# Kernel tuning notes

Hardware: AMD Instinct MI355X
Metric: run time of the kernel (lower is better)

## Reference

```python
import jax, jax.numpy as jnp
import numpy as np

N0, N1, N2, N3 = 200000, 100000, 50000, 25000
E0, E1, E2 = 1600000, 800000, 400000
IN_DIM, HID = 16, 128


def setup_inputs() -> dict:
    key = jax.random.key(0)
    ks = jax.random.split(key, 12)
    inp = {
        "features": jax.random.normal(ks[0], (N0, IN_DIM), jnp.float32),
        "W_init": jax.random.normal(ks[1], (IN_DIM, HID), jnp.float32) / np.sqrt(IN_DIM),
        "b_init": jnp.zeros((HID,), jnp.float32),
        "W_self": jax.random.normal(ks[2], (HID, HID), jnp.float32) / np.sqrt(HID),
        "b_self": jnp.zeros((HID,), jnp.float32),
        "W_neigh": jax.random.normal(ks[3], (HID, HID), jnp.float32) / np.sqrt(HID),
        "b_neigh": jnp.zeros((HID,), jnp.float32),
        "src0": jax.random.randint(ks[4], (E0,), 0, N0, jnp.int32),
        "dst0": jax.random.randint(ks[5], (E0,), 0, N1, jnp.int32),
        "src1": jax.random.randint(ks[6], (E1,), 0, N1, jnp.int32),
        "dst1": jax.random.randint(ks[7], (E1,), 0, N2, jnp.int32),
        "src2": jax.random.randint(ks[8], (E2,), 0, N2, jnp.int32),
        "dst2": jax.random.randint(ks[9], (E2,), 0, N3, jnp.int32),
        "n1": N1, "n2": N2, "n3": N3,
    }
    return inp


def _mean_agg(h_src, src, dst, n_out):
    # gather messages along edges, segment-mean into dst nodes
    msg = h_src[src]                                             # [E, HID]
    agg = jax.ops.segment_sum(msg, dst, num_segments=n_out)      # [n_out, HID]
    cnt = jax.ops.segment_sum(jnp.ones_like(dst, jnp.float32), dst, num_segments=n_out)
    return agg / jnp.maximum(cnt, 1.0)[:, None]


def reference(features, W_init, b_init, W_self, b_self, W_neigh, b_neigh,
              src0, dst0, src1, dst1, src2, dst2, n1, n2, n3):
    # h = activation(fc_init(features))
    h = jax.nn.relu(features @ W_init + b_init)                  # [N0, HID]
    blocks = [(src0, dst0, n1), (src1, dst1, n2), (src2, dst2, n3)]
    depth = len(blocks)
    for i, (src, dst, n_out) in enumerate(blocks):
        h_neigh = _mean_agg(h, src, dst, n_out)
        # SAGEConv mean, combine_type='sum': fc_self(h_dst) + fc_neigh(mean_neigh)
        h = (h[:n_out] @ W_self + b_self) + (h_neigh @ W_neigh + b_neigh)
        if i != depth - 1:
            h = jax.nn.relu(h)
    return h                                                     # [N3, HID]
```

## Files before the change

### kernel.cpp

```cpp
#include <hip/hip_runtime.h>

#define HID 128
#define CAP 64
#define NCB 49
#define TILE 1024
#define CCAP0 40960
#define CCAP1 20480
#define CCAP2 10240

typedef __attribute__((ext_vector_type(2))) _Float16 h2v;
typedef __attribute__((ext_vector_type(8))) _Float16 f16x8;
typedef __attribute__((ext_vector_type(4))) float f32x4;

__global__ __launch_bounds__(256) void h0_and_bin(
        const float* __restrict__ feat, const float* __restrict__ W_init,
        const float* __restrict__ b_init, _Float16* __restrict__ h0, int M, int nh0blk,
        const int* __restrict__ src0, const int* __restrict__ dst0, int E0,
        const int* __restrict__ src1, const int* __restrict__ dst1, int E1,
        const int* __restrict__ src2, const int* __restrict__ dst2, int E2,
        int* __restrict__ gcur,
        int* __restrict__ buf0, int* __restrict__ buf1, int* __restrict__ buf2,
        int nb0, int nb1, int nb2) {
    __shared__ int hist[NCB];
    __shared__ int gbase[NCB];
    const int nbTot = nb0 + nb1 + nb2;
    if (blockIdx.x < (unsigned)nbTot) {
        const int* src; const int* dst; int E, SH, lb, nblk, ccap; int* buf; int* cur;
        int b = blockIdx.x;
        if (b < nb0)             { src = src0; dst = dst0; E = E0; SH = 11; lb = b;             nblk = nb0; buf = buf0; cur = gcur;           ccap = CCAP0; }
        else if (b < nb0 + nb1)  { src = src1; dst = dst1; E = E1; SH = 10; lb = b - nb0;       nblk = nb1; buf = buf1; cur = gcur + NCB;     ccap = CCAP1; }
        else                     { src = src2; dst = dst2; E = E2; SH = 9;  lb = b - nb0 - nb1; nblk = nb2; buf = buf2; cur = gcur + 2 * NCB; ccap = CCAP2; }
        const int ntile = (E + TILE - 1) / TILE;
        for (int t = lb; t < ntile; t += nblk) {
            const int base = t * TILE;
            const int n = min(TILE, E - base);
            for (int i = threadIdx.x; i < NCB; i += 256) hist[i] = 0;
            __syncthreads();
            int eb[4], er[4], ee[4];
#pragma unroll
            for (int k = 0; k < 4; k++) {
                int idx = k * 256 + threadIdx.x;
                eb[k] = -1;
                if (idx < n) {
                    int d = dst[base + idx], s = src[base + idx];
                    int bb = d >> SH;
                    eb[k] = bb;
                    ee[k] = ((d - (bb << SH)) << 18) | s;
                    er[k] = atomicAdd(&hist[bb], 1);
                }
            }
            __syncthreads();
            if (threadIdx.x < NCB)
                gbase[threadIdx.x] = atomicAdd(&cur[threadIdx.x], hist[threadIdx.x]);
            __syncthreads();
#pragma unroll
            for (int k = 0; k < 4; k++) {
                if (eb[k] >= 0) {
                    int pos = gbase[eb[k]] + er[k];
                    if (pos < ccap) buf[(size_t)eb[k] * ccap + pos] = ee[k];
                }
            }
            __syncthreads();
        }
        return;
    }
    const int hbid = blockIdx.x - nbTot;
    const int tid  = threadIdx.x;
    const int lane = tid & 63;
    const int wave = tid >> 6;
    const int ln15 = lane & 15;
    const int quad = lane >> 4;

    f16x8 Bf[2];
    float bias[2];
#pragma unroll
    for (int cc = 0; cc < 2; cc++) {
        int n = (wave * 2 + cc) * 16 + ln15;
        bias[cc] = b_init[n];
        f16x8 b;
#pragma unroll
        for (int jj = 0; jj < 8; jj++) {
            int k = quad * 8 + jj;
            b[jj] = (k < 16) ? (_Float16)W_init[k * HID + n] : (_Float16)0.f;
        }
        Bf[cc] = b;
    }

    for (int row0 = hbid * 16; row0 < M; row0 += nh0blk * 16) {
        const int arow = row0 + ln15;
        f16x8 A = {0, 0, 0, 0, 0, 0, 0, 0};
        if (arow < M && quad < 2) {
            const float* p = feat + (size_t)arow * 16 + quad * 8;
            float4 v0 = *(const float4*)p;
            float4 v1 = *(const float4*)(p + 4);
            A[0] = (_Float16)v0.x; A[1] = (_Float16)v0.y;
            A[2] = (_Float16)v0.z; A[3] = (_Float16)v0.w;
            A[4] = (_Float16)v1.x; A[5] = (_Float16)v1.y;
            A[6] = (_Float16)v1.z; A[7] = (_Float16)v1.w;
        }
        f32x4 acc0 = {0.f, 0.f, 0.f, 0.f};
        f32x4 acc1 = {0.f, 0.f, 0.f, 0.f};
        acc0 = __builtin_amdgcn_mfma_f32_16x16x32_f16(A, Bf[0], acc0, 0, 0, 0);
        acc1 = __builtin_amdgcn_mfma_f32_16x16x32_f16(A, Bf[1], acc1, 0, 0, 0);
#pragma unroll
        for (int cc = 0; cc < 2; cc++) {
            int col = (wave * 2 + cc) * 16 + ln15;
            f32x4 acc = cc ? acc1 : acc0;
#pragma unroll
            for (int r = 0; r < 4; r++) {
                int row = row0 + quad * 4 + r;
                if (row < M)
                    h0[(size_t)row * HID + col] = (_Float16)fmaxf(acc[r] + bias[cc], 0.f);
            }
        }
    }
}

__global__ __launch_bounds__(1024) void refine_coarse(
        const int* __restrict__ buf0, const int* __restrict__ buf1, const int* __restrict__ buf2,
        const int* __restrict__ gcur, int* __restrict__ csrcur,
        int N1v, int N2v, int N3v,
        int* __restrict__ csr0, int* __restrict__ off0, int* __restrict__ cnt0,
        int* __restrict__ csr1, int* __restrict__ off1, int* __restrict__ cnt1,
        int* __restrict__ csr2, int* __restrict__ off2, int* __restrict__ cnt2) {
    __shared__ int hist[2048];
    __shared__ int loff[2048];
    __shared__ int wsum[16];
    __shared__ int blkbase;
    const int tid = threadIdx.x;
    const int gb = blockIdx.x;
    const int* buf; int* csr; int* off; int* cnt; int* ccur;
    int SH, N, bb, ccap, m;
    if (gb < NCB)          { buf = buf0; csr = csr0; off = off0; cnt = cnt0; ccur = csrcur;     SH = 11; N = N1v; bb = gb;           ccap = CCAP0; }
    else if (gb < 2 * NCB) { buf = buf1; csr = csr1; off = off1; cnt = cnt1; ccur = csrcur + 1; SH = 10; N = N2v; bb = gb - NCB;     ccap = CCAP1; }
    else                   { buf = buf2; csr = csr2; off = off2; cnt = cnt2; ccur = csrcur + 2; SH = 9;  N = N3v; bb = gb - 2 * NCB; ccap = CCAP2; }
    m = min(gcur[gb], ccap);
    const int* __restrict__ seg = buf + (size_t)bb * ccap;
    const int nb_d = 1 << SH;
    for (int i = tid; i < 2048; i += 1024) hist[i] = 0;
    __syncthreads();
    for (int i = tid; i < m; i += 1024)
        atomicAdd(&hist[((unsigned)seg[i]) >> 18], 1);
    __syncthreads();
    int v0 = hist[2 * tid], v1 = hist[2 * tid + 1];
    int s = v0 + v1;
    int lane = tid & 63;
    int incl = s;
#pragma unroll
    for (int d = 1; d < 64; d <<= 1) {
        int up = __shfl_up(incl, d, 64);
        if (lane >= d) incl += up;
    }
    if (lane == 63) wsum[tid >> 6] = incl;
    __syncthreads();
    if (tid == 0) {
        int acc = 0;
#pragma unroll
        for (int i = 0; i < 16; i++) { int w = wsum[i]; wsum[i] = acc; acc += w; }
        blkbase = atomicAdd(ccur, acc);
    }
    __syncthreads();
    int base = blkbase + wsum[tid >> 6] + (incl - s);
    loff[2 * tid] = base;
    loff[2 * tid + 1] = base + v0;
    const int dbase = bb << SH;
    {
        int dl0 = 2 * tid, dl1 = 2 * tid + 1;
        if (dl0 < nb_d && dbase + dl0 < N) { off[dbase + dl0] = base;      cnt[dbase + dl0] = v0; }
        if (dl1 < nb_d && dbase + dl1 < N) { off[dbase + dl1] = base + v0; cnt[dbase + dl1] = v1; }
    }
    __syncthreads();
    for (int i = tid; i < 2048; i += 1024) hist[i] = 0;
    __syncthreads();
    for (int i = tid; i < m; i += 1024) {
        int e = seg[i];
        int dl = ((unsigned)e) >> 18;
        int p = atomicAdd(&hist[dl], 1);
        csr[loff[dl] + p] = e & 0x3FFFF;
    }
}

__device__ __forceinline__ void acc8(float* s, uint4 u) {
    union { uint4 u; h2v p[4]; } w; w.u = u;
#pragma unroll
    for (int q = 0; q < 4; q++) {
        s[2 * q]     += (float)w.p[q][0];
        s[2 * q + 1] += (float)w.p[q][1];
    }
}

__global__ __launch_bounds__(256) void gather_mean(
        const _Float16* __restrict__ h,
        const int* __restrict__ csr,
        const int* __restrict__ off,
        const int* __restrict__ cnt,
        _Float16* __restrict__ Xm,
        int n_out) {
    const int g = threadIdx.x >> 4;
    const int c = threadIdx.x & 15;
    const int node = blockIdx.x * 16 + g;
    if (node >= n_out) return;
    int deg = min(cnt[node], CAP);
    const int* __restrict__ sl = csr + off[node];
    float s[8] = {0.f, 0.f, 0.f, 0.f, 0.f, 0.f, 0.f, 0.f};
    int e = 0;
    for (; e + 8 <= deg; e += 8) {
        uint4 R[8];
#pragma unroll
        for (int k = 0; k < 8; k++)
            R[k] = *(const uint4*)(h + (size_t)sl[e + k] * HID + c * 8);
#pragma unroll
        for (int k = 0; k < 8; k++) acc8(s, R[k]);
    }
    if (e + 4 <= deg) {
        uint4 R[4];
#pragma unroll
        for (int k = 0; k < 4; k++)
            R[k] = *(const uint4*)(h + (size_t)sl[e + k] * HID + c * 8);
#pragma unroll
        for (int k = 0; k < 4; k++) acc8(s, R[k]);
        e += 4;
    }
    for (; e < deg; e++)
        acc8(s, *(const uint4*)(h + (size_t)sl[e] * HID + c * 8));
    float inv = 1.0f / (float)max(deg, 1);
    union { uint4 u; h2v p[4]; } mo;
#pragma unroll
    for (int q = 0; q < 4; q++)
        mo.p[q] = (h2v){(_Float16)(s[2 * q] * inv), (_Float16)(s[2 * q + 1] * inv)};
    *(uint4*)(Xm + (size_t)node * HID + c * 8) = mo.u;
}

template <bool RELU, typename OutT>
__global__ __launch_bounds__(256) void mfma_combine2(
        const _Float16* __restrict__ Hself, const _Float16* __restrict__ Xm,
        const float* __restrict__ Wself, const float* __restrict__ bself,
        const float* __restrict__ Wneigh, const float* __restrict__ bneigh,
        OutT* __restrict__ out, int M) {
    const int tid  = threadIdx.x;
    const int lane = tid & 63;
    const int wave = tid >> 6;
    const int ln15 = lane & 15;
    const int quad = lane >> 4;

    f16x8 Bf[2][8];
    float bias[2];
#pragma unroll
    for (int cc = 0; cc < 2; cc++) {
        int n = (wave * 2 + cc) * 16 + ln15;
        bias[cc] = bself[n] + bneigh[n];
#pragma unroll
        for (int s = 0; s < 8; s++) {
            f16x8 b;
#pragma unroll
            for (int jj = 0; jj < 8; jj++) {
                int k = s * 32 + quad * 8 + jj;
                float w = (k < HID) ? Wself[k * HID + n] : Wneigh[(k - HID) * HID + n];
                b[jj] = (_Float16)w;
            }
            Bf[cc][s] = b;
        }
    }

    for (int row0 = blockIdx.x * 16; row0 < M; row0 += gridDim.x * 16) {
        const int arow = row0 + ln15;
        const bool inb = arow < M;
        const _Float16* aps = Hself + (size_t)arow * HID + quad * 8;
        const _Float16* apm = Xm    + (size_t)arow * HID + quad * 8;
        f32x4 acc0 = {0.f, 0.f, 0.f, 0.f};
        f32x4 acc1 = {0.f, 0.f, 0.f, 0.f};
#pragma unroll
        for (int s = 0; s < 8; s++) {
            f16x8 A;
            if (inb) A = (s < 4) ? *(const f16x8*)(aps + s * 32)
                                 : *(const f16x8*)(apm + (s - 4) * 32);
            else     A = (f16x8){0, 0, 0, 0, 0, 0, 0, 0};
            acc0 = __builtin_amdgcn_mfma_f32_16x16x32_f16(A, Bf[0][s], acc0, 0, 0, 0);
            acc1 = __builtin_amdgcn_mfma_f32_16x16x32_f16(A, Bf[1][s], acc1, 0, 0, 0);
        }
#pragma unroll
        for (int cc = 0; cc < 2; cc++) {
            int col = (wave * 2 + cc) * 16 + ln15;
            f32x4 acc = cc ? acc1 : acc0;
#pragma unroll
            for (int r = 0; r < 4; r++) {
                int row = row0 + quad * 4 + r;
                if (row < M) {
                    float v = acc[r] + bias[cc];
                    if (RELU) v = fmaxf(v, 0.f);
                    out[(size_t)row * HID + col] = (OutT)v;
                }
            }
        }
    }
}

extern "C" void kernel_launch(void* const* d_in, const int* in_sizes, int n_in,
                              void* d_out, int out_size, void* d_ws, size_t ws_size,
                              hipStream_t stream) {
    const float* feat    = (const float*)d_in[0];
    const float* W_init  = (const float*)d_in[1];
    const float* b_init  = (const float*)d_in[2];
    const float* W_self  = (const float*)d_in[3];
    const float* b_self  = (const float*)d_in[4];
    const float* W_neigh = (const float*)d_in[5];
    const float* b_neigh = (const float*)d_in[6];
    const int* src0 = (const int*)d_in[7];
    const int* dst0 = (const int*)d_in[8];
    const int* src1 = (const int*)d_in[9];
    const int* dst1 = (const int*)d_in[10];
    const int* src2 = (const int*)d_in[11];
    const int* dst2 = (const int*)d_in[12];

    const int N0 = in_sizes[0] / 16;
    const int E0 = in_sizes[7];
    const int E1 = in_sizes[9];
    const int E2 = in_sizes[11];
    const int N1 = 100000, N2 = 50000, N3 = 25000;

    _Float16* h0 = (_Float16*)d_ws;
    _Float16* hA = h0 + (size_t)N0 * HID;
    int* csr0 = (int*)(hA + (size_t)N1 * HID);
    int* csr1 = csr0 + E0;
    int* csr2 = csr1 + E1;
    int* off0 = csr2 + E2;
    int* off1 = off0 + N1;
    int* off2 = off1 + N2;
    int* cnt0 = off2 + N3;
    int* cnt1 = cnt0 + N1;
    int* cnt2 = cnt1 + N2;
    int* gcur = cnt2 + N3;
    int* csrcur = gcur + 3 * NCB;
    int* buf0 = csrcur + 3;
    int* buf1 = buf0 + (size_t)NCB * CCAP0;
    int* buf2 = buf1 + (size_t)NCB * CCAP1;
    _Float16* Xm = (_Float16*)buf0;
    _Float16* hB = h0;

    hipMemsetAsync(gcur, 0, (3 * NCB + 3) * sizeof(int), stream);

    const int nb0 = 768, nb1 = 384, nb2 = 192, nh0blk = 3136;
    h0_and_bin<<<nb0 + nb1 + nb2 + nh0blk, 256, 0, stream>>>(
        feat, W_init, b_init, h0, N0, nh0blk,
        src0, dst0, E0, src1, dst1, E1, src2, dst2, E2,
        gcur, buf0, buf1, buf2, nb0, nb1, nb2);
    refine_coarse<<<3 * NCB, 1024, 0, stream>>>(
        buf0, buf1, buf2, gcur, csrcur, N1, N2, N3,
        csr0, off0, cnt0, csr1, off1, cnt1, csr2, off2, cnt2);

    gather_mean<<<(N1 + 15) / 16, 256, 0, stream>>>(h0, csr0, off0, cnt0, Xm, N1);
    mfma_combine2<true, _Float16><<<min((N1 + 15) / 16, 1568), 256, 0, stream>>>(
        h0, Xm, W_self, b_self, W_neigh, b_neigh, hA, N1);
    gather_mean<<<(N2 + 15) / 16, 256, 0, stream>>>(hA, csr1, off1, cnt1, Xm, N2);
    mfma_combine2<true, _Float16><<<min((N2 + 15) / 16, 1568), 256, 0, stream>>>(
        hA, Xm, W_self, b_self, W_neigh, b_neigh, hB, N2);
    gather_mean<<<(N3 + 15) / 16, 256, 0, stream>>>(hB, csr2, off2, cnt2, Xm, N3);
    mfma_combine2<false, float><<<min((N3 + 15) / 16, 1568), 256, 0, stream>>>(
        hB, Xm, W_self, b_self, W_neigh, b_neigh, (float*)d_out, N3);
}
```

Baseline: 402.5 us.

## Build CSR via global count, scan and atomic scatter instead of bucket sort

Replaces the two-stage coarse-bucket binning plus per-bucket LDS refine with a three-kernel CSR build. The first kernel counts in-degrees with global atomics, the second does an exclusive-scan into cursors, and the third scatters src ids into CSR slots with returning global atomicSub. The initial feature projection also moves from MFMA to plain fp32 FMA per output column, fused into the counting kernel. This removes the large staging buffers and one full pass over the edges. The cost is millions of random returning global atomics and nondeterministic neighbor order within each row.

```diff
diff --git a/kernel.cpp b/kernel.cpp
--- a/kernel.cpp
+++ b/kernel.cpp
@@ -2,148 +2,84 @@
 
 #define HID 128
 #define CAP 64
-#define NCB 49
-#define TILE 1024
-#define CCAP0 40960
-#define CCAP1 20480
-#define CCAP2 10240
 
 typedef __attribute__((ext_vector_type(2))) _Float16 h2v;
 typedef __attribute__((ext_vector_type(8))) _Float16 f16x8;
 typedef __attribute__((ext_vector_type(4))) float f32x4;
 
-__global__ __launch_bounds__(256) void h0_and_bin(
+__global__ __launch_bounds__(256) void h0_and_count(
         const float* __restrict__ feat, const float* __restrict__ W_init,
-        const float* __restrict__ b_init, _Float16* __restrict__ h0, int M, int nh0blk,
-        const int* __restrict__ src0, const int* __restrict__ dst0, int E0,
-        const int* __restrict__ src1, const int* __restrict__ dst1, int E1,
-        const int* __restrict__ src2, const int* __restrict__ dst2, int E2,
-        int* __restrict__ gcur,
-        int* __restrict__ buf0, int* __restrict__ buf1, int* __restrict__ buf2,
-        int nb0, int nb1, int nb2) {
-    __shared__ int hist[NCB];
-    __shared__ int gbase[NCB];
-    const int nbTot = nb0 + nb1 + nb2;
-    if (blockIdx.x < (unsigned)nbTot) {
-        const int* src; const int* dst; int E, SH, lb, nblk, ccap; int* buf; int* cur;
-        int b = blockIdx.x;
-        if (b < nb0)             { src = src0; dst = dst0; E = E0; SH = 11; lb = b;             nblk = nb0; buf = buf0; cur = gcur;           ccap = CCAP0; }
-        else if (b < nb0 + nb1)  { src = src1; dst = dst1; E = E1; SH = 10; lb = b - nb0;       nblk = nb1; buf = buf1; cur = gcur + NCB;     ccap = CCAP1; }
-        else                     { src = src2; dst = dst2; E = E2; SH = 9;  lb = b - nb0 - nb1; nblk = nb2; buf = buf2; cur = gcur + 2 * NCB; ccap = CCAP2; }
-        const int ntile = (E + TILE - 1) / TILE;
-        for (int t = lb; t < ntile; t += nblk) {
-            const int base = t * TILE;
-            const int n = min(TILE, E - base);
-            for (int i = threadIdx.x; i < NCB; i += 256) hist[i] = 0;
-            __syncthreads();
-            int eb[4], er[4], ee[4];
-#pragma unroll
-            for (int k = 0; k < 4; k++) {
-                int idx = k * 256 + threadIdx.x;
-                eb[k] = -1;
-                if (idx < n) {
-                    int d = dst[base + idx], s = src[base + idx];
-                    int bb = d >> SH;
-                    eb[k] = bb;
-                    ee[k] = ((d - (bb << SH)) << 18) | s;
-                    er[k] = atomicAdd(&hist[bb], 1);
-                }
+        const float* __restrict__ b_init, _Float16* __restrict__ h0, int M,
+        int nCnt, int nH0,
+        const int* __restrict__ dst0, int E0,
+        const int* __restrict__ dst1, int E1,
+        const int* __restrict__ dst2, int E2,
+        int* __restrict__ cnt0, int* __restrict__ cnt1, int* __restrict__ cnt2) {
+    const int b = blockIdx.x;
+    if (b < nCnt) {
+        const int nc0 = nCnt / 2, nc1 = nCnt / 4;
+        const int* dst; int* cnt; int E, lb, nb;
+        if (b < nc0)            { dst = dst0; cnt = cnt0; E = E0; lb = b;             nb = nc0; }
+        else if (b < nc0 + nc1) { dst = dst1; cnt = cnt1; E = E1; lb = b - nc0;       nb = nc1; }
+        else                    { dst = dst2; cnt = cnt2; E = E2; lb = b - nc0 - nc1; nb = nCnt - nc0 - nc1; }
+        const int n4 = E >> 2;
+        for (int i = lb * 256 + threadIdx.x; i < n4; i += nb * 256) {
+            int4 d = ((const int4*)dst)[i];
+            atomicAdd(&cnt[d.x], 1);
+            atomicAdd(&cnt[d.y], 1);
+            atomicAdd(&cnt[d.z], 1);
+            atomicAdd(&cnt[d.w], 1);
+        }
+        if (lb == 0) {
+            int t = (E & ~3) + threadIdx.x;
+            if (t < E) atomicAdd(&cnt[dst[t]], 1);
+        }
+        return;
+    }
+    const int hb = b - nCnt;
+    const int j  = threadIdx.x & 127;
+    const int rl = threadIdx.x >> 7;
+    float Wc[16];
+#pragma unroll
+    for (int k = 0; k < 16; k++) Wc[k] = W_init[k * HID + j];
+    const float bi = b_init[j];
+    for (int r0 = hb * 8; r0 < M; r0 += nH0 * 8) {
+        float4 F[4][4];
+#pragma unroll
+        for (int u = 0; u < 4; u++) {
+            int row = r0 + u * 2 + rl;
+            if (row < M) {
+                const float4* p = (const float4*)(feat + (size_t)row * 16);
+                F[u][0] = p[0]; F[u][1] = p[1]; F[u][2] = p[2]; F[u][3] = p[3];
             }
-            __syncthreads();
-            if (threadIdx.x < NCB)
-                gbase[threadIdx.x] = atomicAdd(&cur[threadIdx.x], hist[threadIdx.x]);
-            __syncthreads();
-#pragma unroll
-            for (int k = 0; k < 4; k++) {
-                if (eb[k] >= 0) {
-                    int pos = gbase[eb[k]] + er[k];
-                    if (pos < ccap) buf[(size_t)eb[k] * ccap + pos] = ee[k];
-                }
-            }
-            __syncthreads();
-        }
-        return;
-    }
-    const int hbid = blockIdx.x - nbTot;
-    const int tid  = threadIdx.x;
-    const int lane = tid & 63;
-    const int wave = tid >> 6;
-    const int ln15 = lane & 15;
-    const int quad = lane >> 4;
-
-    f16x8 Bf[2];
-    float bias[2];
-#pragma unroll
-    for (int cc = 0; cc < 2; cc++) {
-        int n = (wave * 2 + cc) * 16 + ln15;
-        bias[cc] = b_init[n];
-        f16x8 b;
-#pragma unroll
-        for (int jj = 0; jj < 8; jj++) {
-            int k = quad * 8 + jj;
-            b[jj] = (k < 16) ? (_Float16)W_init[k * HID + n] : (_Float16)0.f;
-        }
-        Bf[cc] = b;
-    }
-
-    for (int row0 = hbid * 16; row0 < M; row0 += nh0blk * 16) {
-        const int arow = row0 + ln15;
-        f16x8 A = {0, 0, 0, 0, 0, 0, 0, 0};
-        if (arow < M && quad < 2) {
-            const float* p = feat + (size_t)arow * 16 + quad * 8;
-            float4 v0 = *(const float4*)p;
-            float4 v1 = *(const float4*)(p + 4);
-            A[0] = (_Float16)v0.x; A[1] = (_Float16)v0.y;
-            A[2] = (_Float16)v0.z; A[3] = (_Float16)v0.w;
-            A[4] = (_Float16)v1.x; A[5] = (_Float16)v1.y;
-            A[6] = (_Float16)v1.z; A[7] = (_Float16)v1.w;
-        }
-        f32x4 acc0 = {0.f, 0.f, 0.f, 0.f};
-        f32x4 acc1 = {0.f, 0.f, 0.f, 0.f};
-        acc0 = __builtin_amdgcn_mfma_f32_16x16x32_f16(A, Bf[0], acc0, 0, 0, 0);
-        acc1 = __builtin_amdgcn_mfma_f32_16x16x32_f16(A, Bf[1], acc1, 0, 0, 0);
-#pragma unroll
-        for (int cc = 0; cc < 2; cc++) {
-            int col = (wave * 2 + cc) * 16 + ln15;
-            f32x4 acc = cc ? acc1 : acc0;
-#pragma unroll
-            for (int r = 0; r < 4; r++) {
-                int row = row0 + quad * 4 + r;
-                if (row < M)
-                    h0[(size_t)row * HID + col] = (_Float16)fmaxf(acc[r] + bias[cc], 0.f);
-            }
-        }
-    }
-}
-
-__global__ __launch_bounds__(1024) void refine_coarse(
-        const int* __restrict__ buf0, const int* __restrict__ buf1, const int* __restrict__ buf2,
-        const int* __restrict__ gcur, int* __restrict__ csrcur,
-        int N1v, int N2v, int N3v,
-        int* __restrict__ csr0, int* __restrict__ off0, int* __restrict__ cnt0,
-        int* __restrict__ csr1, int* __restrict__ off1, int* __restrict__ cnt1,
-        int* __restrict__ csr2, int* __restrict__ off2, int* __restrict__ cnt2) {
-    __shared__ int hist[2048];
-    __shared__ int loff[2048];
-    __shared__ int wsum[16];
-    __shared__ int blkbase;
+        }
+#pragma unroll
+        for (int u = 0; u < 4; u++) {
+            int row = r0 + u * 2 + rl;
+            if (row >= M) continue;
+            const float* f = (const float*)&F[u][0];
+            float a = bi;
+#pragma unroll
+            for (int k = 0; k < 16; k++) a = fmaf(f[k], Wc[k], a);
+            h0[(size_t)row * HID + j] = (_Float16)fmaxf(a, 0.f);
+        }
+    }
+}
+
+__global__ __launch_bounds__(1024) void scan_cur(
+        const int* __restrict__ cnt0, const int* __restrict__ cnt1, const int* __restrict__ cnt2,
+        int* __restrict__ cur0, int* __restrict__ cur1, int* __restrict__ cur2,
+        int N1v, int N2v, int N3v, int nb1, int nb2, int* __restrict__ gb) {
+    const int b = blockIdx.x;
+    const int* cnt; int* cur; int N, lb; int* g;
+    if (b < nb1)            { cnt = cnt0; cur = cur0; N = N1v; lb = b;             g = gb;     }
+    else if (b < nb1 + nb2) { cnt = cnt1; cur = cur1; N = N2v; lb = b - nb1;       g = gb + 1; }
+    else                    { cnt = cnt2; cur = cur2; N = N3v; lb = b - nb1 - nb2; g = gb + 2; }
     const int tid = threadIdx.x;
-    const int gb = blockIdx.x;
-    const int* buf; int* csr; int* off; int* cnt; int* ccur;
-    int SH, N, bb, ccap, m;
-    if (gb < NCB)          { buf = buf0; csr = csr0; off = off0; cnt = cnt0; ccur = csrcur;     SH = 11; N = N1v; bb = gb;           ccap = CCAP0; }
-    else if (gb < 2 * NCB) { buf = buf1; csr = csr1; off = off1; cnt = cnt1; ccur = csrcur + 1; SH = 10; N = N2v; bb = gb - NCB;     ccap = CCAP1; }
-    else                   { buf = buf2; csr = csr2; off = off2; cnt = cnt2; ccur = csrcur + 2; SH = 9;  N = N3v; bb = gb - 2 * NCB; ccap = CCAP2; }
-    m = min(gcur[gb], ccap);
-    const int* __restrict__ seg = buf + (size_t)bb * ccap;
-    const int nb_d = 1 << SH;
-    for (int i = tid; i < 2048; i += 1024) hist[i] = 0;
-    __syncthreads();
-    for (int i = tid; i < m; i += 1024)
-        atomicAdd(&hist[((unsigned)seg[i]) >> 18], 1);
-    __syncthreads();
-    int v0 = hist[2 * tid], v1 = hist[2 * tid + 1];
-    int s = v0 + v1;
+    const int base = lb * 4096 + tid * 4;
+    int v[4]; int s = 0;
+#pragma unroll
+    for (int k = 0; k < 4; k++) { v[k] = (base + k < N) ? cnt[base + k] : 0; s += v[k]; }
     int lane = tid & 63;
     int incl = s;
 #pragma unroll
@@ -151,32 +87,52 @@
         int up = __shfl_up(incl, d, 64);
         if (lane >= d) incl += up;
     }
+    __shared__ int wsum[16];
+    __shared__ int bbase;
     if (lane == 63) wsum[tid >> 6] = incl;
     __syncthreads();
     if (tid == 0) {
         int acc = 0;
 #pragma unroll
         for (int i = 0; i < 16; i++) { int w = wsum[i]; wsum[i] = acc; acc += w; }
-        blkbase = atomicAdd(ccur, acc);
+        bbase = atomicAdd(g, acc);
     }
     __syncthreads();
-    int base = blkbase + wsum[tid >> 6] + (incl - s);
-    loff[2 * tid] = base;
-    loff[2 * tid + 1] = base + v0;
-    const int dbase = bb << SH;
-    {
-        int dl0 = 2 * tid, dl1 = 2 * tid + 1;
-        if (dl0 < nb_d && dbase + dl0 < N) { off[dbase + dl0] = base;      cnt[dbase + dl0] = v0; }
-        if (dl1 < nb_d && dbase + dl1 < N) { off[dbase + dl1] = base + v0; cnt[dbase + dl1] = v1; }
-    }
-    __syncthreads();
-    for (int i = tid; i < 2048; i += 1024) hist[i] = 0;
-    __syncthreads();
-    for (int i = tid; i < m; i += 1024) {
-        int e = seg[i];
-        int dl = ((unsigned)e) >> 18;
-        int p = atomicAdd(&hist[dl], 1);
-        csr[loff[dl] + p] = e & 0x3FFFF;
+    int run = bbase + wsum[tid >> 6] + (incl - s);
+#pragma unroll
+    for (int k = 0; k < 4; k++) {
+        run += v[k];
+        if (base + k < N) cur[base + k] = run;
+    }
+}
+
+__global__ __launch_bounds__(256) void scatter_csr(
+        const int* __restrict__ src0, const int* __restrict__ dst0, int E0,
+        const int* __restrict__ src1, const int* __restrict__ dst1, int E1,
+        const int* __restrict__ src2, const int* __restrict__ dst2, int E2,
+        int* __restrict__ cur0, int* __restrict__ cur1, int* __restrict__ cur2,
+        int* __restrict__ csr0, int* __restrict__ csr1, int* __restrict__ csr2,
+        int nc0, int nc1, int nc2) {
+    const int b = blockIdx.x;
+    const int *src, *dst; int *cur, *csr; int E, lb, nb;
+    if (b < nc0)            { src = src0; dst = dst0; cur = cur0; csr = csr0; E = E0; lb = b;             nb = nc0; }
+    else if (b < nc0 + nc1) { src = src1; dst = dst1; cur = cur1; csr = csr1; E = E1; lb = b - nc0;       nb = nc1; }
+    else                    { src = src2; dst = dst2; cur = cur2; csr = csr2; E = E2; lb = b - nc0 - nc1; nb = nc2; }
+    const int n4 = E >> 2;
+    for (int i = lb * 256 + threadIdx.x; i < n4; i += nb * 256) {
+        int4 d = ((const int4*)dst)[i];
+        int4 s = ((const int4*)src)[i];
+        int p0 = atomicSub(&cur[d.x], 1) - 1; csr[p0] = s.x;
+        int p1 = atomicSub(&cur[d.y], 1) - 1; csr[p1] = s.y;
+        int p2 = atomicSub(&cur[d.z], 1) - 1; csr[p2] = s.z;
+        int p3 = atomicSub(&cur[d.w], 1) - 1; csr[p3] = s.w;
+    }
+    if (lb == 0) {
+        int t = (E & ~3) + threadIdx.x;
+        if (t < E) {
+            int p = atomicSub(&cur[dst[t]], 1) - 1;
+            csr[p] = src[t];
+        }
     }
 }
 
@@ -319,42 +275,43 @@
     const int N1 = 100000, N2 = 50000, N3 = 25000;
 
     _Float16* h0 = (_Float16*)d_ws;
-    _Float16* hA = h0 + (size_t)N0 * HID;
-    int* csr0 = (int*)(hA + (size_t)N1 * HID);
-    int* csr1 = csr0 + E0;
+    _Float16* Xm = h0 + (size_t)N0 * HID;
+    int* csr1 = (int*)(Xm + (size_t)N1 * HID);
     int* csr2 = csr1 + E1;
-    int* off0 = csr2 + E2;
-    int* off1 = off0 + N1;
-    int* off2 = off1 + N2;
-    int* cnt0 = off2 + N3;
+    int* cnt0 = csr2 + E2;
     int* cnt1 = cnt0 + N1;
     int* cnt2 = cnt1 + N2;
-    int* gcur = cnt2 + N3;
-    int* csrcur = gcur + 3 * NCB;
-    int* buf0 = csrcur + 3;
-    int* buf1 = buf0 + (size_t)NCB * CCAP0;
-    int* buf2 = buf1 + (size_t)NCB * CCAP1;
-    _Float16* Xm = (_Float16*)buf0;
+    int* gb   = cnt2 + N3;
+    int* cur0 = gb + 16;
+    int* cur1 = cur0 + N1;
+    int* cur2 = cur1 + N2;
+    int* csr0 = cur2 + N3;
+    _Float16* hA = (_Float16*)csr0;
     _Float16* hB = h0;
 
-    hipMemsetAsync(gcur, 0, (3 * NCB + 3) * sizeof(int), stream);
-
-    const int nb0 = 768, nb1 = 384, nb2 = 192, nh0blk = 3136;
-    h0_and_bin<<<nb0 + nb1 + nb2 + nh0blk, 256, 0, stream>>>(
-        feat, W_init, b_init, h0, N0, nh0blk,
+    hipMemsetAsync(cnt0, 0, (size_t)(N1 + N2 + N3 + 16) * sizeof(int), stream);
+
+    const int nCnt = 896, nH0 = 3200;
+    h0_and_count<<<nCnt + nH0, 256, 0, stream>>>(
+        feat, W_init, b_init, h0, N0, nCnt, nH0,
+        dst0, E0, dst1, E1, dst2, E2, cnt0, cnt1, cnt2);
+
+    const int nb1 = (N1 + 4095) / 4096, nb2 = (N2 + 4095) / 4096, nb3 = (N3 + 4095) / 4096;
+    scan_cur<<<nb1 + nb2 + nb3, 1024, 0, stream>>>(
+        cnt0, cnt1, cnt2, cur0, cur1, cur2, N1, N2, N3, nb1, nb2, gb);
+
+    const int ns0 = 768, ns1 = 384, ns2 = 192;
+    scatter_csr<<<ns0 + ns1 + ns2, 256, 0, stream>>>(
         src0, dst0, E0, src1, dst1, E1, src2, dst2, E2,
-        gcur, buf0, buf1, buf2, nb0, nb1, nb2);
-    refine_coarse<<<3 * NCB, 1024, 0, stream>>>(
-        buf0, buf1, buf2, gcur, csrcur, N1, N2, N3,
-        csr0, off0, cnt0, csr1, off1, cnt1, csr2, off2, cnt2);
-
-    gather_mean<<<(N1 + 15) / 16, 256, 0, stream>>>(h0, csr0, off0, cnt0, Xm, N1);
+        cur0, cur1, cur2, csr0, csr1, csr2, ns0, ns1, ns2);
+
+    gather_mean<<<(N1 + 15) / 16, 256, 0, stream>>>(h0, csr0, cur0, cnt0, Xm, N1);
     mfma_combine2<true, _Float16><<<min((N1 + 15) / 16, 1568), 256, 0, stream>>>(
         h0, Xm, W_self, b_self, W_neigh, b_neigh, hA, N1);
-    gather_mean<<<(N2 + 15) / 16, 256, 0, stream>>>(hA, csr1, off1, cnt1, Xm, N2);
+    gather_mean<<<(N2 + 15) / 16, 256, 0, stream>>>(hA, csr1, cur1, cnt1, Xm, N2);
     mfma_combine2<true, _Float16><<<min((N2 + 15) / 16, 1568), 256, 0, stream>>>(
         hA, Xm, W_self, b_self, W_neigh, b_neigh, hB, N2);
-    gather_mean<<<(N3 + 15) / 16, 256, 0, stream>>>(hB, csr2, off2, cnt2, Xm, N3);
+    gather_mean<<<(N3 + 15) / 16, 256, 0, stream>>>(hB, csr2, cur2, cnt2, Xm, N3);
     mfma_combine2<false, float><<<min((N3 + 15) / 16, 1568), 256, 0, stream>>>(
         hB, Xm, W_self, b_self, W_neigh, b_neigh, (float*)d_out, N3);
 }
```

Result: slower. 695.4 us (+72.8%).

## Fuse neighbor gather-mean into MFMA combine kernel via shared-memory tile

Applied to the files above, without the earlier changes.

Merges the per-layer gather_mean and mfma_combine2 kernels into one persistent gather_combine kernel. Each block gathers the neighbor mean for 16 nodes into a shared-memory tile and feeds it straight to the MFMA matmul, so the Xm intermediate never goes to global memory and three launches are removed. It also doubles the edge-binning tile to 2048 edges per iteration. The trade-off is that the fused kernel serializes gather and matmul phases within each block with extra barriers and caps the grid at 1568 blocks, which may lower the number of gathers in flight.

```diff
diff --git a/kernel.cpp b/kernel.cpp
--- a/kernel.cpp
+++ b/kernel.cpp
@@ -3,7 +3,7 @@
 #define HID 128
 #define CAP 64
 #define NCB 49
-#define TILE 1024
+#define TILE 2048
 #define CCAP0 40960
 #define CCAP1 20480
 #define CCAP2 10240
@@ -36,9 +36,9 @@
             const int n = min(TILE, E - base);
             for (int i = threadIdx.x; i < NCB; i += 256) hist[i] = 0;
             __syncthreads();
-            int eb[4], er[4], ee[4];
-#pragma unroll
-            for (int k = 0; k < 4; k++) {
+            int eb[8], er[8], ee[8];
+#pragma unroll
+            for (int k = 0; k < 8; k++) {
                 int idx = k * 256 + threadIdx.x;
                 eb[k] = -1;
                 if (idx < n) {
@@ -54,7 +54,7 @@
                 gbase[threadIdx.x] = atomicAdd(&cur[threadIdx.x], hist[threadIdx.x]);
             __syncthreads();
 #pragma unroll
-            for (int k = 0; k < 4; k++) {
+            for (int k = 0; k < 8; k++) {
                 if (eb[k] >= 0) {
                     int pos = gbase[eb[k]] + er[k];
                     if (pos < ccap) buf[(size_t)eb[k] * ccap + pos] = ee[k];
@@ -189,59 +189,23 @@
     }
 }
 
-__global__ __launch_bounds__(256) void gather_mean(
+template <bool RELU, typename OutT>
+__global__ __launch_bounds__(256) void gather_combine(
         const _Float16* __restrict__ h,
         const int* __restrict__ csr,
         const int* __restrict__ off,
         const int* __restrict__ cnt,
-        _Float16* __restrict__ Xm,
-        int n_out) {
-    const int g = threadIdx.x >> 4;
-    const int c = threadIdx.x & 15;
-    const int node = blockIdx.x * 16 + g;
-    if (node >= n_out) return;
-    int deg = min(cnt[node], CAP);
-    const int* __restrict__ sl = csr + off[node];
-    float s[8] = {0.f, 0.f, 0.f, 0.f, 0.f, 0.f, 0.f, 0.f};
-    int e = 0;
-    for (; e + 8 <= deg; e += 8) {
-        uint4 R[8];
-#pragma unroll
-        for (int k = 0; k < 8; k++)
-            R[k] = *(const uint4*)(h + (size_t)sl[e + k] * HID + c * 8);
-#pragma unroll
-        for (int k = 0; k < 8; k++) acc8(s, R[k]);
-    }
-    if (e + 4 <= deg) {
-        uint4 R[4];
-#pragma unroll
-        for (int k = 0; k < 4; k++)
-            R[k] = *(const uint4*)(h + (size_t)sl[e + k] * HID + c * 8);
-#pragma unroll
-        for (int k = 0; k < 4; k++) acc8(s, R[k]);
-        e += 4;
-    }
-    for (; e < deg; e++)
-        acc8(s, *(const uint4*)(h + (size_t)sl[e] * HID + c * 8));
-    float inv = 1.0f / (float)max(deg, 1);
-    union { uint4 u; h2v p[4]; } mo;
-#pragma unroll
-    for (int q = 0; q < 4; q++)
-        mo.p[q] = (h2v){(_Float16)(s[2 * q] * inv), (_Float16)(s[2 * q + 1] * inv)};
-    *(uint4*)(Xm + (size_t)node * HID + c * 8) = mo.u;
-}
-
-template <bool RELU, typename OutT>
-__global__ __launch_bounds__(256) void mfma_combine2(
-        const _Float16* __restrict__ Hself, const _Float16* __restrict__ Xm,
         const float* __restrict__ Wself, const float* __restrict__ bself,
         const float* __restrict__ Wneigh, const float* __restrict__ bneigh,
-        OutT* __restrict__ out, int M) {
+        OutT* __restrict__ out, int M, int nblk) {
+    __shared__ uint4 Xt[16][17];
     const int tid  = threadIdx.x;
     const int lane = tid & 63;
     const int wave = tid >> 6;
     const int ln15 = lane & 15;
     const int quad = lane >> 4;
+    const int g = tid >> 4;
+    const int c = tid & 15;
 
     f16x8 Bf[2][8];
     float bias[2];
@@ -262,36 +226,77 @@
         }
     }
 
-    for (int row0 = blockIdx.x * 16; row0 < M; row0 += gridDim.x * 16) {
-        const int arow = row0 + ln15;
-        const bool inb = arow < M;
-        const _Float16* aps = Hself + (size_t)arow * HID + quad * 8;
-        const _Float16* apm = Xm    + (size_t)arow * HID + quad * 8;
-        f32x4 acc0 = {0.f, 0.f, 0.f, 0.f};
-        f32x4 acc1 = {0.f, 0.f, 0.f, 0.f};
-#pragma unroll
-        for (int s = 0; s < 8; s++) {
-            f16x8 A;
-            if (inb) A = (s < 4) ? *(const f16x8*)(aps + s * 32)
-                                 : *(const f16x8*)(apm + (s - 4) * 32);
-            else     A = (f16x8){0, 0, 0, 0, 0, 0, 0, 0};
-            acc0 = __builtin_amdgcn_mfma_f32_16x16x32_f16(A, Bf[0][s], acc0, 0, 0, 0);
-            acc1 = __builtin_amdgcn_mfma_f32_16x16x32_f16(A, Bf[1][s], acc1, 0, 0, 0);
-        }
-#pragma unroll
-        for (int cc = 0; cc < 2; cc++) {
-            int col = (wave * 2 + cc) * 16 + ln15;
-            f32x4 acc = cc ? acc1 : acc0;
-#pragma unroll
-            for (int r = 0; r < 4; r++) {
-                int row = row0 + quad * 4 + r;
-                if (row < M) {
-                    float v = acc[r] + bias[cc];
-                    if (RELU) v = fmaxf(v, 0.f);
-                    out[(size_t)row * HID + col] = (OutT)v;
-                }
-            }
-        }
+    for (int row0 = blockIdx.x * 16; row0 < M; row0 += nblk * 16) {
+        {
+            const int node = row0 + g;
+            union { uint4 u; h2v p[4]; } mo;
+            mo.u = (uint4){0, 0, 0, 0};
+            if (node < M) {
+                int deg = min(cnt[node], CAP);
+                const int* __restrict__ sl = csr + off[node];
+                float s[8] = {0.f, 0.f, 0.f, 0.f, 0.f, 0.f, 0.f, 0.f};
+                int e = 0;
+                for (; e + 8 <= deg; e += 8) {
+                    uint4 R[8];
+#pragma unroll
+                    for (int k = 0; k < 8; k++)
+                        R[k] = *(const uint4*)(h + (size_t)sl[e + k] * HID + c * 8);
+#pragma unroll
+                    for (int k = 0; k < 8; k++) acc8(s, R[k]);
+                }
+                if (e + 4 <= deg) {
+                    uint4 R[4];
+#pragma unroll
+                    for (int k = 0; k < 4; k++)
+                        R[k] = *(const uint4*)(h + (size_t)sl[e + k] * HID + c * 8);
+#pragma unroll
+                    for (int k = 0; k < 4; k++) acc8(s, R[k]);
+                    e += 4;
+                }
+                for (; e < deg; e++)
+                    acc8(s, *(const uint4*)(h + (size_t)sl[e] * HID + c * 8));
+                float inv = 1.0f / (float)max(deg, 1);
+#pragma unroll
+                for (int q = 0; q < 4; q++)
+                    mo.p[q] = (h2v){(_Float16)(s[2 * q] * inv), (_Float16)(s[2 * q + 1] * inv)};
+            }
+            Xt[g][c] = mo.u;
+        }
+        __syncthreads();
+        {
+            const int arow = row0 + ln15;
+            const bool inb = arow < M;
+            const _Float16* aps = h + (size_t)arow * HID + quad * 8;
+            f32x4 acc0 = {0.f, 0.f, 0.f, 0.f};
+            f32x4 acc1 = {0.f, 0.f, 0.f, 0.f};
+#pragma unroll
+            for (int s = 0; s < 8; s++) {
+                f16x8 A;
+                if (s < 4) {
+                    if (inb) A = *(const f16x8*)(aps + s * 32);
+                    else     A = (f16x8){0, 0, 0, 0, 0, 0, 0, 0};
+                } else {
+                    A = *(const f16x8*)&Xt[ln15][(s - 4) * 4 + quad];
+                }
+                acc0 = __builtin_amdgcn_mfma_f32_16x16x32_f16(A, Bf[0][s], acc0, 0, 0, 0);
+                acc1 = __builtin_amdgcn_mfma_f32_16x16x32_f16(A, Bf[1][s], acc1, 0, 0, 0);
+            }
+#pragma unroll
+            for (int cc = 0; cc < 2; cc++) {
+                int col = (wave * 2 + cc) * 16 + ln15;
+                f32x4 acc = cc ? acc1 : acc0;
+#pragma unroll
+                for (int r = 0; r < 4; r++) {
+                    int row = row0 + quad * 4 + r;
+                    if (row < M) {
+                        float v = acc[r] + bias[cc];
+                        if (RELU) v = fmaxf(v, 0.f);
+                        out[(size_t)row * HID + col] = (OutT)v;
+                    }
+                }
+            }
+        }
+        __syncthreads();
     }
 }
 
@@ -334,7 +339,6 @@
     int* buf0 = csrcur + 3;
     int* buf1 = buf0 + (size_t)NCB * CCAP0;
     int* buf2 = buf1 + (size_t)NCB * CCAP1;
-    _Float16* Xm = (_Float16*)buf0;
     _Float16* hB = h0;
 
     hipMemsetAsync(gcur, 0, (3 * NCB + 3) * sizeof(int), stream);
@@ -348,13 +352,19 @@
         buf0, buf1, buf2, gcur, csrcur, N1, N2, N3,
         csr0, off0, cnt0, csr1, off1, cnt1, csr2, off2, cnt2);
 
-    gather_mean<<<(N1 + 15) / 16, 256, 0, stream>>>(h0, csr0, off0, cnt0, Xm, N1);
-    mfma_combine2<true, _Float16><<<min((N1 + 15) / 16, 1568), 256, 0, stream>>>(
-        h0, Xm, W_self, b_self, W_neigh, b_neigh, hA, N1);
-    gather_mean<<<(N2 + 15) / 16, 256, 0, stream>>>(hA, csr1, off1, cnt1, Xm, N2);
-    mfma_combine2<true, _Float16><<<min((N2 + 15) / 16, 1568), 256, 0, stream>>>(
-        hA, Xm, W_self, b_self, W_neigh, b_neigh, hB, N2);
-    gather_mean<<<(N3 + 15) / 16, 256, 0, stream>>>(hB, csr2, off2, cnt2, Xm, N3);
-    mfma_combine2<false, float><<<min((N3 + 15) / 16, 1568), 256, 0, stream>>>(
-        hB, Xm, W_self, b_self, W_neigh, b_neigh, (float*)d_out, N3);
-}
+    {
+        int g = min((N1 + 15) / 16, 1568);
+        gather_combine<true, _Float16><<<g, 256, 0, stream>>>(
+            h0, csr0, off0, cnt0, W_self, b_self, W_neigh, b_neigh, hA, N1, g);
+    }
+    {
+        int g = min((N2 + 15) / 16, 1568);
+        gather_combine<true, _Float16><<<g, 256, 0, stream>>>(
+            hA, csr1, off1, cnt1, W_self, b_self, W_neigh, b_neigh, hB, N2, g);
+    }
+    {
+        int g = min((N3 + 15) / 16, 1568);
+        gather_combine<false, float><<<g, 256, 0, stream>>>(
+            hB, csr2, off2, cnt2, W_self, b_self, W_neigh, b_neigh, (float*)d_out, N3, g);
+    }
+}
```

Result: no change. 408.1 us (+1.4%).

## Split edge binning into finer sub-buckets and fuse CSR refine with h0

Applied to the files above, without the earlier changes.

Edge binning now uses 512-node coarse buckets, each split into 8 per-block sub-buckets, with 2048-edge tiles. The CSR refine step therefore runs on 343 smaller 512-thread blocks instead of 147 1024-thread blocks, and contention on the global bucket cursors is lower. The h0 input projection moves out of the binning kernel and into the refine kernel so it overlaps with the refine work. The combine layers now write in place into one feature buffer, with a block barrier added before the stores. The fixed per-sub-bucket capacity can silently drop edges if a sub-bucket overflows.

```diff
diff --git a/kernel.cpp b/kernel.cpp
--- a/kernel.cpp
+++ b/kernel.cpp
@@ -2,72 +2,141 @@
 
 #define HID 128
 #define CAP 64
-#define NCB 49
-#define TILE 1024
-#define CCAP0 40960
-#define CCAP1 20480
-#define CCAP2 10240
+#define SHB 9
+#define NCB0 196
+#define NCB1 98
+#define NCB2 49
+#define SUB 8
+#define CS 1280
+#define TILE 2048
 
 typedef __attribute__((ext_vector_type(2))) _Float16 h2v;
 typedef __attribute__((ext_vector_type(8))) _Float16 f16x8;
 typedef __attribute__((ext_vector_type(4))) float f32x4;
 
-__global__ __launch_bounds__(256) void h0_and_bin(
-        const float* __restrict__ feat, const float* __restrict__ W_init,
-        const float* __restrict__ b_init, _Float16* __restrict__ h0, int M, int nh0blk,
+__global__ __launch_bounds__(256) void bin_coarse(
         const int* __restrict__ src0, const int* __restrict__ dst0, int E0,
         const int* __restrict__ src1, const int* __restrict__ dst1, int E1,
         const int* __restrict__ src2, const int* __restrict__ dst2, int E2,
         int* __restrict__ gcur,
         int* __restrict__ buf0, int* __restrict__ buf1, int* __restrict__ buf2,
         int nb0, int nb1, int nb2) {
-    __shared__ int hist[NCB];
-    __shared__ int gbase[NCB];
-    const int nbTot = nb0 + nb1 + nb2;
-    if (blockIdx.x < (unsigned)nbTot) {
-        const int* src; const int* dst; int E, SH, lb, nblk, ccap; int* buf; int* cur;
-        int b = blockIdx.x;
-        if (b < nb0)             { src = src0; dst = dst0; E = E0; SH = 11; lb = b;             nblk = nb0; buf = buf0; cur = gcur;           ccap = CCAP0; }
-        else if (b < nb0 + nb1)  { src = src1; dst = dst1; E = E1; SH = 10; lb = b - nb0;       nblk = nb1; buf = buf1; cur = gcur + NCB;     ccap = CCAP1; }
-        else                     { src = src2; dst = dst2; E = E2; SH = 9;  lb = b - nb0 - nb1; nblk = nb2; buf = buf2; cur = gcur + 2 * NCB; ccap = CCAP2; }
-        const int ntile = (E + TILE - 1) / TILE;
-        for (int t = lb; t < ntile; t += nblk) {
-            const int base = t * TILE;
-            const int n = min(TILE, E - base);
-            for (int i = threadIdx.x; i < NCB; i += 256) hist[i] = 0;
-            __syncthreads();
-            int eb[4], er[4], ee[4];
-#pragma unroll
-            for (int k = 0; k < 4; k++) {
-                int idx = k * 256 + threadIdx.x;
-                eb[k] = -1;
-                if (idx < n) {
-                    int d = dst[base + idx], s = src[base + idx];
-                    int bb = d >> SH;
-                    eb[k] = bb;
-                    ee[k] = ((d - (bb << SH)) << 18) | s;
-                    er[k] = atomicAdd(&hist[bb], 1);
-                }
-            }
-            __syncthreads();
-            if (threadIdx.x < NCB)
-                gbase[threadIdx.x] = atomicAdd(&cur[threadIdx.x], hist[threadIdx.x]);
-            __syncthreads();
-#pragma unroll
-            for (int k = 0; k < 4; k++) {
-                if (eb[k] >= 0) {
-                    int pos = gbase[eb[k]] + er[k];
-                    if (pos < ccap) buf[(size_t)eb[k] * ccap + pos] = ee[k];
-                }
-            }
-            __syncthreads();
+    __shared__ int hist[NCB0];
+    __shared__ int gbase[NCB0];
+    const int* src; const int* dst; int E, lb, nblk, ncb; int* buf; int* cur;
+    int b = blockIdx.x;
+    if (b < nb0)             { src = src0; dst = dst0; E = E0; lb = b;             nblk = nb0; buf = buf0; cur = gcur;                          ncb = NCB0; }
+    else if (b < nb0 + nb1)  { src = src1; dst = dst1; E = E1; lb = b - nb0;       nblk = nb1; buf = buf1; cur = gcur + NCB0 * SUB;             ncb = NCB1; }
+    else                     { src = src2; dst = dst2; E = E2; lb = b - nb0 - nb1; nblk = nb2; buf = buf2; cur = gcur + (NCB0 + NCB1) * SUB;    ncb = NCB2; }
+    const int sub = lb & (SUB - 1);
+    const int ntile = (E + TILE - 1) / TILE;
+    for (int t = lb; t < ntile; t += nblk) {
+        const int base = t * TILE;
+        const int n = min(TILE, E - base);
+        for (int i = threadIdx.x; i < ncb; i += 256) hist[i] = 0;
+        __syncthreads();
+        int eb[8], er[8], ee[8];
+#pragma unroll
+        for (int k = 0; k < 8; k++) {
+            int idx = k * 256 + threadIdx.x;
+            eb[k] = -1;
+            if (idx < n) {
+                int d = dst[base + idx], s = src[base + idx];
+                int bb = d >> SHB;
+                eb[k] = bb;
+                ee[k] = ((d & 511) << 18) | s;
+                er[k] = atomicAdd(&hist[bb], 1);
+            }
+        }
+        __syncthreads();
+        for (int i = threadIdx.x; i < ncb; i += 256)
+            gbase[i] = atomicAdd(&cur[i * SUB + sub], hist[i]);
+        __syncthreads();
+#pragma unroll
+        for (int k = 0; k < 8; k++) {
+            if (eb[k] >= 0) {
+                int pos = gbase[eb[k]] + er[k];
+                if (pos < CS) buf[((size_t)eb[k] * SUB + sub) * CS + pos] = ee[k];
+            }
+        }
+        __syncthreads();
+    }
+}
+
+__global__ __launch_bounds__(512) void refine_h0(
+        const int* __restrict__ buf0, const int* __restrict__ buf1, const int* __restrict__ buf2,
+        const int* __restrict__ gcur, int* __restrict__ csrcur,
+        int N1v, int N2v, int N3v, int nRef,
+        int* __restrict__ csr0, int* __restrict__ off0, int* __restrict__ cnt0,
+        int* __restrict__ csr1, int* __restrict__ off1, int* __restrict__ cnt1,
+        int* __restrict__ csr2, int* __restrict__ off2, int* __restrict__ cnt2,
+        const float* __restrict__ feat, const float* __restrict__ W_init,
+        const float* __restrict__ b_init, _Float16* __restrict__ h0, int M, int nh0) {
+    __shared__ int hist[512];
+    __shared__ int loff[512];
+    __shared__ int wsum[8];
+    __shared__ int blkbase;
+    const int tid = threadIdx.x;
+    if (blockIdx.x < (unsigned)nRef) {
+        const int gb = blockIdx.x;
+        const int* buf; int* csr; int* off; int* cnt; int* ccur; const int* cur;
+        int N, bb;
+        if (gb < NCB0)            { buf = buf0; csr = csr0; off = off0; cnt = cnt0; ccur = csrcur;     cur = gcur;                       N = N1v; bb = gb; }
+        else if (gb < NCB0 + NCB1){ buf = buf1; csr = csr1; off = off1; cnt = cnt1; ccur = csrcur + 1; cur = gcur + NCB0 * SUB;          N = N2v; bb = gb - NCB0; }
+        else                      { buf = buf2; csr = csr2; off = off2; cnt = cnt2; ccur = csrcur + 2; cur = gcur + (NCB0 + NCB1) * SUB; N = N3v; bb = gb - NCB0 - NCB1; }
+        int m[SUB];
+#pragma unroll
+        for (int j = 0; j < SUB; j++) m[j] = min(cur[bb * SUB + j], CS);
+        hist[tid] = 0;
+        __syncthreads();
+#pragma unroll
+        for (int j = 0; j < SUB; j++) {
+            const int* __restrict__ seg = buf + ((size_t)bb * SUB + j) * CS;
+            for (int i = tid; i < m[j]; i += 512)
+                atomicAdd(&hist[((unsigned)seg[i]) >> 18], 1);
+        }
+        __syncthreads();
+        int v = hist[tid];
+        int lane = tid & 63;
+        int incl = v;
+#pragma unroll
+        for (int d = 1; d < 64; d <<= 1) {
+            int up = __shfl_up(incl, d, 64);
+            if (lane >= d) incl += up;
+        }
+        if (lane == 63) wsum[tid >> 6] = incl;
+        __syncthreads();
+        if (tid == 0) {
+            int acc = 0;
+#pragma unroll
+            for (int i = 0; i < 8; i++) { int w = wsum[i]; wsum[i] = acc; acc += w; }
+            blkbase = atomicAdd(ccur, acc);
+        }
+        __syncthreads();
+        int base = blkbase + wsum[tid >> 6] + (incl - v);
+        loff[tid] = base;
+        const int node = (bb << SHB) + tid;
+        if (node < N) { off[node] = base; cnt[node] = v; }
+        __syncthreads();
+        hist[tid] = 0;
+        __syncthreads();
+#pragma unroll
+        for (int j = 0; j < SUB; j++) {
+            const int* __restrict__ seg = buf + ((size_t)bb * SUB + j) * CS;
+            for (int i = tid; i < m[j]; i += 512) {
+                int e = seg[i];
+                int dl = ((unsigned)e) >> 18;
+                int p = atomicAdd(&hist[dl], 1);
+                csr[loff[dl] + p] = e & 0x3FFFF;
+            }
         }
         return;
     }
-    const int hbid = blockIdx.x - nbTot;
-    const int tid  = threadIdx.x;
-    const int lane = tid & 63;
-    const int wave = tid >> 6;
+    const int hb   = blockIdx.x - nRef;
+    const int sb   = tid >> 8;
+    const int t    = tid & 255;
+    const int lane = t & 63;
+    const int wave = t >> 6;
     const int ln15 = lane & 15;
     const int quad = lane >> 4;
 
@@ -86,7 +155,7 @@
         Bf[cc] = b;
     }
 
-    for (int row0 = hbid * 16; row0 < M; row0 += nh0blk * 16) {
+    for (int row0 = (hb * 2 + sb) * 16; row0 < M; row0 += nh0 * 32) {
         const int arow = row0 + ln15;
         f16x8 A = {0, 0, 0, 0, 0, 0, 0, 0};
         if (arow < M && quad < 2) {
@@ -113,70 +182,6 @@
                     h0[(size_t)row * HID + col] = (_Float16)fmaxf(acc[r] + bias[cc], 0.f);
             }
         }
-    }
-}
-
-__global__ __launch_bounds__(1024) void refine_coarse(
-        const int* __restrict__ buf0, const int* __restrict__ buf1, const int* __restrict__ buf2,
-        const int* __restrict__ gcur, int* __restrict__ csrcur,
-        int N1v, int N2v, int N3v,
-        int* __restrict__ csr0, int* __restrict__ off0, int* __restrict__ cnt0,
-        int* __restrict__ csr1, int* __restrict__ off1, int* __restrict__ cnt1,
-        int* __restrict__ csr2, int* __restrict__ off2, int* __restrict__ cnt2) {
-    __shared__ int hist[2048];
-    __shared__ int loff[2048];
-    __shared__ int wsum[16];
-    __shared__ int blkbase;
-    const int tid = threadIdx.x;
-    const int gb = blockIdx.x;
-    const int* buf; int* csr; int* off; int* cnt; int* ccur;
-    int SH, N, bb, ccap, m;
-    if (gb < NCB)          { buf = buf0; csr = csr0; off = off0; cnt = cnt0; ccur = csrcur;     SH = 11; N = N1v; bb = gb;           ccap = CCAP0; }
-    else if (gb < 2 * NCB) { buf = buf1; csr = csr1; off = off1; cnt = cnt1; ccur = csrcur + 1; SH = 10; N = N2v; bb = gb - NCB;     ccap = CCAP1; }
-    else                   { buf = buf2; csr = csr2; off = off2; cnt = cnt2; ccur = csrcur + 2; SH = 9;  N = N3v; bb = gb - 2 * NCB; ccap = CCAP2; }
-    m = min(gcur[gb], ccap);
-    const int* __restrict__ seg = buf + (size_t)bb * ccap;
-    const int nb_d = 1 << SH;
-    for (int i = tid; i < 2048; i += 1024) hist[i] = 0;
-    __syncthreads();
-    for (int i = tid; i < m; i += 1024)
-        atomicAdd(&hist[((unsigned)seg[i]) >> 18], 1);
-    __syncthreads();
-    int v0 = hist[2 * tid], v1 = hist[2 * tid + 1];
-    int s = v0 + v1;
-    int lane = tid & 63;
-    int incl = s;
-#pragma unroll
-    for (int d = 1; d < 64; d <<= 1) {
-        int up = __shfl_up(incl, d, 64);
-        if (lane >= d) incl += up;
-    }
-    if (lane == 63) wsum[tid >> 6] = incl;
-    __syncthreads();
-    if (tid == 0) {
-        int acc = 0;
-#pragma unroll
-        for (int i = 0; i < 16; i++) { int w = wsum[i]; wsum[i] = acc; acc += w; }
-        blkbase = atomicAdd(ccur, acc);
-    }
-    __syncthreads();
-    int base = blkbase + wsum[tid >> 6] + (incl - s);
-    loff[2 * tid] = base;
-    loff[2 * tid + 1] = base + v0;
-    const int dbase = bb << SH;
-    {
-        int dl0 = 2 * tid, dl1 = 2 * tid + 1;
-        if (dl0 < nb_d && dbase + dl0 < N) { off[dbase + dl0] = base;      cnt[dbase + dl0] = v0; }
-        if (dl1 < nb_d && dbase + dl1 < N) { off[dbase + dl1] = base + v0; cnt[dbase + dl1] = v1; }
-    }
-    __syncthreads();
-    for (int i = tid; i < 2048; i += 1024) hist[i] = 0;
-    __syncthreads();
-    for (int i = tid; i < m; i += 1024) {
-        int e = seg[i];
-        int dl = ((unsigned)e) >> 18;
-        int p = atomicAdd(&hist[dl], 1);
-        csr[loff[dl] + p] = e & 0x3FFFF;
     }
 }
 
@@ -233,10 +238,10 @@
 
 template <bool RELU, typename OutT>
 __global__ __launch_bounds__(256) void mfma_combine2(
-        const _Float16* __restrict__ Hself, const _Float16* __restrict__ Xm,
+        const _Float16* Hself, const _Float16* __restrict__ Xm,
         const float* __restrict__ Wself, const float* __restrict__ bself,
         const float* __restrict__ Wneigh, const float* __restrict__ bneigh,
-        OutT* __restrict__ out, int M) {
+        OutT* out, int M) {
     const int tid  = threadIdx.x;
     const int lane = tid & 63;
     const int wave = tid >> 6;
@@ -278,6 +283,7 @@
             acc0 = __builtin_amdgcn_mfma_f32_16x16x32_f16(A, Bf[0][s], acc0, 0, 0, 0);
             acc1 = __builtin_amdgcn_mfma_f32_16x16x32_f16(A, Bf[1][s], acc1, 0, 0, 0);
         }
+        __syncthreads();
 #pragma unroll
         for (int cc = 0; cc < 2; cc++) {
             int col = (wave * 2 + cc) * 16 + ln15;
@@ -318,9 +324,9 @@
     const int E2 = in_sizes[11];
     const int N1 = 100000, N2 = 50000, N3 = 25000;
 
-    _Float16* h0 = (_Float16*)d_ws;
-    _Float16* hA = h0 + (size_t)N0 * HID;
-    int* csr0 = (int*)(hA + (size_t)N1 * HID);
+    _Float16* h  = (_Float16*)d_ws;
+    _Float16* Xm = h + (size_t)N0 * HID;
+    int* csr0 = (int*)(Xm + (size_t)N1 * HID);
     int* csr1 = csr0 + E0;
     int* csr2 = csr1 + E1;
     int* off0 = csr2 + E2;
@@ -330,31 +336,31 @@
     int* cnt1 = cnt0 + N1;
     int* cnt2 = cnt1 + N2;
     int* gcur = cnt2 + N3;
-    int* csrcur = gcur + 3 * NCB;
+    int* csrcur = gcur + (NCB0 + NCB1 + NCB2) * SUB;
     int* buf0 = csrcur + 3;
-    int* buf1 = buf0 + (size_t)NCB * CCAP0;
-    int* buf2 = buf1 + (size_t)NCB * CCAP1;
-    _Float16* Xm = (_Float16*)buf0;
-    _Float16* hB = h0;
-
-    hipMemsetAsync(gcur, 0, (3 * NCB + 3) * sizeof(int), stream);
-
-    const int nb0 = 768, nb1 = 384, nb2 = 192, nh0blk = 3136;
-    h0_and_bin<<<nb0 + nb1 + nb2 + nh0blk, 256, 0, stream>>>(
-        feat, W_init, b_init, h0, N0, nh0blk,
+    int* buf1 = buf0 + (size_t)NCB0 * SUB * CS;
+    int* buf2 = buf1 + (size_t)NCB1 * SUB * CS;
+
+    hipMemsetAsync(gcur, 0, ((NCB0 + NCB1 + NCB2) * SUB + 3) * sizeof(int), stream);
+
+    const int nb0 = 768, nb1 = 384, nb2 = 192;
+    bin_coarse<<<nb0 + nb1 + nb2, 256, 0, stream>>>(
         src0, dst0, E0, src1, dst1, E1, src2, dst2, E2,
         gcur, buf0, buf1, buf2, nb0, nb1, nb2);
-    refine_coarse<<<3 * NCB, 1024, 0, stream>>>(
-        buf0, buf1, buf2, gcur, csrcur, N1, N2, N3,
-        csr0, off0, cnt0, csr1, off1, cnt1, csr2, off2, cnt2);
-
-    gather_mean<<<(N1 + 15) / 16, 256, 0, stream>>>(h0, csr0, off0, cnt0, Xm, N1);
+
+    const int nRef = NCB0 + NCB1 + NCB2, nh0 = 3072;
+    refine_h0<<<nRef + nh0, 512, 0, stream>>>(
+        buf0, buf1, buf2, gcur, csrcur, N1, N2, N3, nRef,
+        csr0, off0, cnt0, csr1, off1, cnt1, csr2, off2, cnt2,
+        feat, W_init, b_init, h, N0, nh0);
+
+    gather_mean<<<(N1 + 15) / 16, 256, 0, stream>>>(h, csr0, off0, cnt0, Xm, N1);
     mfma_combine2<true, _Float16><<<min((N1 + 15) / 16, 1568), 256, 0, stream>>>(
-        h0, Xm, W_self, b_self, W_neigh, b_neigh, hA, N1);
-    gather_mean<<<(N2 + 15) / 16, 256, 0, stream>>>(hA, csr1, off1, cnt1, Xm, N2);
+        h, Xm, W_self, b_self, W_neigh, b_neigh, h, N1);
+    gather_mean<<<(N2 + 15) / 16, 256, 0, stream>>>(h, csr1, off1, cnt1, Xm, N2);
     mfma_combine2<true, _Float16><<<min((N2 + 15) / 16, 1568), 256, 0, stream>>>(
-        hA, Xm, W_self, b_self, W_neigh, b_neigh, hB, N2);
-    gather_mean<<<(N3 + 15) / 16, 256, 0, stream>>>(hB, csr2, off2, cnt2, Xm, N3);
+        h, Xm, W_self, b_self, W_neigh, b_neigh, h, N2);
+    gather_mean<<<(N3 + 15) / 16, 256, 0, stream>>>(h, csr2, off2, cnt2, Xm, N3);
     mfma_combine2<false, float><<<min((N3 + 15) / 16, 1568), 256, 0, stream>>>(
-        hB, Xm, W_self, b_self, W_neigh, b_neigh, (float*)d_out, N3);
-}
+        h, Xm, W_self, b_self, W_neigh, b_neigh, (float*)d_out, N3);
+}
```

Result: faster. 382.2 us (-5.0%).
